# Kernel optimization log

Hardware: AMD Instinct MI355X
Metric: run time of the kernel (lower is better)

Reference implementation:

```python
import jax, jax.numpy as jnp
import numpy as np


def setup_inputs() -> dict:
    key = jax.random.key(0)
    k1, k2, k3, k4 = jax.random.split(key, 4)
    B, L, D, M = 4, 512, 257, 128
    return {
        "input": jax.random.normal(k1, (B, L, 2), dtype=jnp.float32),
        "z0": jax.random.normal(k2, (D,), dtype=jnp.float32),
        "om": jax.random.uniform(k3, (M, 2), dtype=jnp.float32),
        "S": jax.random.normal(k4, (D, D), dtype=jnp.float32),
    }


def _get_T(x, om, S):
    # x: [B, L, 2], om: [M, 2], S: [D, D] with D = 2M+1
    D = S.shape[0]
    M = om.shape[0]
    k_dot_x = jnp.einsum("blc,mc->blm", x, om)          # [B, L, M]
    c = jnp.cos(k_dot_x)
    s = jnp.sin(k_dot_x)
    B, L = x.shape[0], x.shape[1]
    idx1 = 2 * jnp.arange(M) + 1                          # odd indices
    idx2 = idx1 + 1                                       # even indices
    T_irrep = jnp.zeros((B, L, D, D), dtype=x.dtype)
    T_irrep = T_irrep.at[:, :, 0, 0].set(1.0)             # trivial irrep
    T_irrep = T_irrep.at[:, :, idx1, idx1].set(c)
    T_irrep = T_irrep.at[:, :, idx1, idx2].set(-s)
    T_irrep = T_irrep.at[:, :, idx2, idx1].set(s)
    T_irrep = T_irrep.at[:, :, idx2, idx2].set(c)
    S_inv = jnp.linalg.inv(S)
    # T = S @ T_irrep @ S^-1 for every (b, l)
    T = jnp.einsum("ij,bljk,kn->blin", S, T_irrep, S_inv)
    return T


def reference(input, z0, om, S):
    B = input.shape[0]
    T = _get_T(input, om, S)                              # [B, L, D, D]
    z_init = jnp.broadcast_to(z0, (B, z0.shape[0]))       # [B, D]

    def scan_fn(z, T_t):                                  # T_t: [B, D, D]
        z_new = jnp.einsum("bij,bj->bi", T_t, z)
        return z_new, z_new

    _, outs = jax.lax.scan(scan_fn, z_init, jnp.swapaxes(T, 0, 1))  # [L, B, D]
    outputs = jnp.swapaxes(outs, 0, 1)                    # [B, L, D]
    z_final = outputs[:, -1, :]
    return outputs, z_final
```

## Files before the change

kernel.cpp:

```cpp
#include <hip/hip_runtime.h>
#include <math.h>

#define N    257
#define AP   258
#define MM   128
#define LL   512
#define BB   4
#define NB   32
#define U12S 226

#define A_BYTE    0
#define W0_BYTE   530448
#define CXY_BYTE  531488
#define PW_BYTE   547904
#define U12_BYTE  613696
#define ST_BYTE   671552

__global__ __launch_bounds__(512) void stage_scan_kernel(const float* __restrict__ S,
                                                         const float* __restrict__ z0,
                                                         const float* __restrict__ x,
                                                         void* __restrict__ wsv) {
  const int tid = threadIdx.x;
  const int bid = blockIdx.x;

  if (bid < 130) {
    double* A  = (double*)((char*)wsv + A_BYTE);
    float*  St = (float*)((char*)wsv + ST_BYTE);
    const int idx = bid * 512 + tid;
    if (idx < N * N) {
      const int i = idx / N, j = idx - i * N;
      A[(size_t)i * AP + j] = (double)S[idx];
      St[idx] = S[j * N + i];
    } else if (idx < N * N + N) {
      const int r = idx - N * N;
      A[(size_t)r * AP + N] = (double)z0[r];
    }
    return;
  }

  const int wave = tid >> 6, lane = tid & 63;
  const int b    = wave >> 1, comp = wave & 1;
  const float* xp = x + ((size_t)b * LL) * 2 + comp;
  double loc[8];
  double run = 0.0;
  #pragma unroll
  for (int e = 0; e < 8; ++e) {
    run += (double)xp[(lane * 8 + e) * 2];
    loc[e] = run;
  }
  double tot = run;
  #pragma unroll
  for (int off = 1; off < 64; off <<= 1) {
    const double o = __shfl_up(tot, off);
    if (lane >= off) tot += o;
  }
  const double excl = tot - run;
  float* cp = (float*)((char*)wsv + CXY_BYTE) + ((size_t)b * LL) * 2 + comp;
  #pragma unroll
  for (int e = 0; e < 8; ++e)
    cp[(lane * 8 + e) * 2] = (float)(excl + loc[e]);
}

__global__ __launch_bounds__(320, 1) void panel_factor_kernel(void* __restrict__ wsv,
                                                              int k0) {
  __shared__ double piv[2][NB];
  __shared__ double pinvs[2];
  __shared__ double F11s[NB][NB + 1];
  double* A    = (double*)((char*)wsv + A_BYTE);
  double* Pw   = (double*)((char*)wsv + PW_BYTE);
  double* U12w = (double*)((char*)wsv + U12_BYTE);
  const int tid = threadIdx.x;
  const int ct  = k0 + NB;
  const int tc2 = 258 - ct;

  double r[NB];
  if (tid < N) {
    const double* Ar = A + (size_t)tid * AP + k0;
    #pragma unroll
    for (int c = 0; c < NB; c += 2) {
      const double2 v = *(const double2*)&Ar[c];
      r[c] = v.x; r[c + 1] = v.y;
    }
  }

  if (tid == k0) {
    #pragma unroll
    for (int c = 0; c < NB; ++c) piv[0][c] = r[c];
    pinvs[0] = 1.0 / r[0];
  }
  __syncthreads();

  #pragma unroll
  for (int j = 0; j < NB; ++j) {
    const int pr = k0 + j;
    const int bsel = j & 1;
    if (tid < N && (tid < k0 || tid > pr)) {
      const double f = r[j] * pinvs[bsel];
      #pragma unroll
      for (int j2 = j + 1; j2 < NB; ++j2)
        r[j2] -= f * piv[bsel][j2];
      r[j] = f;
      if (j + 1 < NB && tid == pr + 1) {
        #pragma unroll
        for (int c = 0; c < NB; ++c)
          if (c > j) piv[bsel ^ 1][c] = r[c];
        pinvs[bsel ^ 1] = 1.0 / r[j + 1];
      }
    }
    __syncthreads();
  }

  if (tid < N) {
    if (tid >= k0 && tid < ct) {
      const int fr = tid - k0;
      #pragma unroll
      for (int c = 0; c < NB; ++c) {
        F11s[fr][c] = r[c];
        A[(size_t)tid * AP + k0 + c] = r[c];
      }
    } else {
      #pragma unroll
      for (int t = 0; t < NB; ++t)
        Pw[(size_t)t * N + tid] = r[t];
    }
  }
  __syncthreads();

  if (tid < tc2) {
    double u[NB];
    #pragma unroll
    for (int jr = 0; jr < NB; ++jr)
      u[jr] = A[(size_t)(k0 + jr) * AP + ct + tid];
    #pragma unroll
    for (int jr = 1; jr < NB; ++jr) {
      double vv = u[jr];
      #pragma unroll
      for (int t = 0; t < jr; ++t)
        vv -= F11s[jr][t] * u[t];
      u[jr] = vv;
    }
    #pragma unroll
    for (int jr = 0; jr < NB; ++jr) {
      U12w[jr * U12S + tid] = u[jr];
      A[(size_t)(k0 + jr) * AP + ct + tid] = u[jr];
    }
  }
}

__global__ __launch_bounds__(256) void panel_update_kernel(void* __restrict__ wsv,
                                                           int k0, int tc2) {
  __shared__ double Pl[NB][NB + 1];
  __shared__ __align__(16) double Ul[NB][66];
  double* A = (double*)((char*)wsv + A_BYTE);
  const double* Pw   = (const double*)((const char*)wsv + PW_BYTE);
  const double* U12w = (const double*)((const char*)wsv + U12_BYTE);
  const int tid = threadIdx.x;
  const int ct  = k0 + NB;
  const int rb0 = blockIdx.x * 32;
  const int c0  = blockIdx.y * 64;

  for (int i = tid; i < 32 * 32; i += 256) {
    const int t = i >> 5, rr = i & 31;
    const int rb = rb0 + rr;
    const int gr = (rb < k0) ? rb : rb + NB;
    Pl[t][rr] = (rb < 225) ? Pw[(size_t)t * N + gr] : 0.0;
  }
  for (int i = tid; i < 32 * 64; i += 256) {
    const int t = i >> 6, c = i & 63;
    Ul[t][c] = (c0 + c < tc2) ? U12w[t * U12S + c0 + c] : 0.0;
  }
  __syncthreads();

  const int tr  = tid >> 4;
  const int tcx = (tid & 15) * 4;
  double acc[2][4];
  #pragma unroll
  for (int rr = 0; rr < 2; ++rr) {
    const int rb = rb0 + tr * 2 + rr;
    const int gr = (rb < k0) ? rb : rb + NB;
    #pragma unroll
    for (int c = 0; c < 4; ++c)
      acc[rr][c] = (rb < 225 && (c0 + tcx + c) < tc2)
                 ? A[(size_t)gr * AP + ct + c0 + tcx + c] : 0.0;
  }
  #pragma unroll
  for (int t = 0; t < NB; ++t) {
    const double p0 = Pl[t][tr * 2], p1 = Pl[t][tr * 2 + 1];
    const double2 u0 = *(const double2*)&Ul[t][tcx];
    const double2 u1 = *(const double2*)&Ul[t][tcx + 2];
    acc[0][0] -= p0 * u0.x; acc[0][1] -= p0 * u0.y;
    acc[0][2] -= p0 * u1.x; acc[0][3] -= p0 * u1.y;
    acc[1][0] -= p1 * u0.x; acc[1][1] -= p1 * u0.y;
    acc[1][2] -= p1 * u1.x; acc[1][3] -= p1 * u1.y;
  }
  #pragma unroll
  for (int rr = 0; rr < 2; ++rr) {
    const int rb = rb0 + tr * 2 + rr;
    const int gr = (rb < k0) ? rb : rb + NB;
    #pragma unroll
    for (int c = 0; c < 4; ++c)
      if (rb < 225 && (c0 + tcx + c) < tc2)
        A[(size_t)gr * AP + ct + c0 + tcx + c] = acc[rr][c];
  }
}

__global__ __launch_bounds__(256) void last_kernel(void* __restrict__ wsv) {
  __shared__ double xs[N];
  __shared__ double rr[256];
  double* A = (double*)((char*)wsv + A_BYTE);
  const double* Pw   = (const double*)((const char*)wsv + PW_BYTE);
  const double* U12w = (const double*)((const char*)wsv + U12_BYTE);
  float* w0f = (float*)((char*)wsv + W0_BYTE);
  const int tid = threadIdx.x;

  for (int idx = tid; idx < 225 * 2; idx += 256) {
    const int rb = idx >> 1, c = idx & 1;
    const int gr = (rb < 224) ? rb : 256;
    double acc = A[(size_t)gr * AP + 256 + c];
    #pragma unroll
    for (int t = 0; t < NB; ++t)
      acc -= Pw[(size_t)t * N + gr] * U12w[t * U12S + c];
    A[(size_t)gr * AP + 256 + c] = acc;
  }
  __threadfence_block();
  __syncthreads();

  if (tid == 0) xs[256] = A[256 * AP + 257] / A[256 * AP + 256];
  __syncthreads();
  const double x256 = xs[256];
  rr[tid] = A[(size_t)tid * AP + 257] - A[(size_t)tid * AP + 256] * x256;
  __syncthreads();
  const int fk0 = tid & ~31;
  const int fs  = tid & 31;
  for (int j = 31; j >= 0; --j) {
    if (fs == j) xs[fk0 + j] = rr[fk0 + j] / A[(size_t)(fk0 + j) * AP + (fk0 + j)];
    __syncthreads();
    if (fs < j) rr[fk0 + fs] -= A[(size_t)(fk0 + fs) * AP + (fk0 + j)] * xs[fk0 + j];
    __syncthreads();
  }
  w0f[tid] = (float)xs[tid];
  if (tid == 0) w0f[256] = (float)xs[256];
}

#define NL 8
__global__ __launch_bounds__(320) void combine_kernel(const float* __restrict__ S,
                                                      const float* __restrict__ om,
                                                      const void* __restrict__ wsv,
                                                      float* __restrict__ out) {
  const int tid = threadIdx.x;
  const int b  = blockIdx.y;
  const int l0 = blockIdx.x * NL;
  const float* w0  = (const float*)((const char*)wsv + W0_BYTE);
  const float* cxy = (const float*)((const char*)wsv + CXY_BYTE);
  const float* St  = (const float*)((const char*)wsv + ST_BYTE);
  __shared__ __align__(16) float Wl[N][NL];
  __shared__ float omsh[2 * MM];
  __shared__ float cxs[NL], cys[NL];

  for (int idx = tid; idx < 2 * MM; idx += 320) omsh[idx] = om[idx];
  if (tid < NL) {
    cxs[tid] = cxy[((size_t)(b * LL) + l0 + tid) * 2];
    cys[tid] = cxy[((size_t)(b * LL) + l0 + tid) * 2 + 1];
  }
  __syncthreads();

  for (int idx = tid; idx < NL * N; idx += 320) {
    const int d = idx >> 3;
    const int r = idx & 7;
    float v;
    if (d == 0) {
      v = w0[0];
    } else {
      const int m = (d - 1) >> 1;
      const int pq = 2 * m + 1;
      const float t = cxs[r] * omsh[2 * m] + cys[r] * omsh[2 * m + 1];
      float s, c;
      sincosf(t, &s, &c);
      const float a0 = w0[pq], a1 = w0[pq + 1];
      v = (d & 1) ? (c * a0 - s * a1) : (s * a0 + c * a1);
    }
    Wl[d][r] = v;
  }
  __syncthreads();

  const int i = tid;
  if (i < N) {
    float acc[NL];
    #pragma unroll
    for (int r = 0; r < NL; ++r) acc[r] = 0.0f;
    #pragma unroll 8
    for (int d = 0; d < N; ++d) {
      const float stv = St[(size_t)d * N + i];
      const float4 wa = *(const float4*)&Wl[d][0];
      const float4 wb = *(const float4*)&Wl[d][4];
      acc[0] += stv * wa.x; acc[1] += stv * wa.y;
      acc[2] += stv * wa.z; acc[3] += stv * wa.w;
      acc[4] += stv * wb.x; acc[5] += stv * wb.y;
      acc[6] += stv * wb.z; acc[7] += stv * wb.w;
    }
    const size_t base = (size_t)(b * LL + l0) * N + i;
    #pragma unroll
    for (int r = 0; r < NL; ++r) out[base + (size_t)r * N] = acc[r];
    if (l0 + NL == LL) {
      out[(size_t)BB * LL * N + (size_t)b * N + i] = acc[NL - 1];
    }
  }
}

extern "C" void kernel_launch(void* const* d_in, const int* in_sizes, int n_in,
                              void* d_out, int out_size, void* d_ws, size_t ws_size,
                              hipStream_t stream) {
  const float* x  = (const float*)d_in[0];
  const float* z0 = (const float*)d_in[1];
  const float* om = (const float*)d_in[2];
  const float* S  = (const float*)d_in[3];
  float* out = (float*)d_out;

  hipLaunchKernelGGL(stage_scan_kernel, dim3(131), dim3(512), 0, stream, S, z0, x, d_ws);
  for (int p = 0; p < 8; ++p) {
    const int k0  = p * NB;
    const int tc2 = 258 - (k0 + NB);
    hipLaunchKernelGGL(panel_factor_kernel, dim3(1), dim3(320), 0, stream, d_ws, k0);
    if (p < 7)
      hipLaunchKernelGGL(panel_update_kernel, dim3(8, (tc2 + 63) / 64), dim3(256),
                         0, stream, d_ws, k0, tc2);
  }
  hipLaunchKernelGGL(last_kernel, dim3(1), dim3(256), 0, stream, d_ws);
  hipLaunchKernelGGL(combine_kernel, dim3(LL / NL, BB), dim3(320), 0, stream, S, om, d_ws, out);
}
```

Baseline: 345.3 us.

## Factor diagonal panel block with wavefront shuffles instead of per-column block barriers

New measurement: 567.3 us. +64.3%, slower.

```diff
diff --git a/kernel.cpp b/kernel.cpp
--- a/kernel.cpp
+++ b/kernel.cpp
@@ -63,9 +63,8 @@
 
 __global__ __launch_bounds__(320, 1) void panel_factor_kernel(void* __restrict__ wsv,
                                                               int k0) {
-  __shared__ double piv[2][NB];
-  __shared__ double pinvs[2];
   __shared__ double F11s[NB][NB + 1];
+  __shared__ double pinv[NB];
   double* A    = (double*)((char*)wsv + A_BYTE);
   double* Pw   = (double*)((char*)wsv + PW_BYTE);
   double* U12w = (double*)((char*)wsv + U12_BYTE);
@@ -73,9 +72,18 @@
   const int ct  = k0 + NB;
   const int tc2 = 258 - ct;
 
+  int myrow;
+  if (tid < 64) {
+    myrow = k0 + tid;
+  } else {
+    const int rr = tid - 64;
+    myrow = (rr < k0) ? rr : rr + 64;
+  }
+  const bool act = myrow < N;
+
   double r[NB];
-  if (tid < N) {
-    const double* Ar = A + (size_t)tid * AP + k0;
+  if (act) {
+    const double* Ar = A + (size_t)myrow * AP + k0;
     #pragma unroll
     for (int c = 0; c < NB; c += 2) {
       const double2 v = *(const double2*)&Ar[c];
@@ -83,66 +91,64 @@
     }
   }
 
-  if (tid == k0) {
-    #pragma unroll
-    for (int c = 0; c < NB; ++c) piv[0][c] = r[c];
-    pinvs[0] = 1.0 / r[0];
-  }
-  __syncthreads();
-
-  #pragma unroll
-  for (int j = 0; j < NB; ++j) {
-    const int pr = k0 + j;
-    const int bsel = j & 1;
-    if (tid < N && (tid < k0 || tid > pr)) {
-      const double f = r[j] * pinvs[bsel];
+  if (tid < 64) {
+    #pragma unroll
+    for (int j = 0; j < NB; ++j) {
+      const double ujj = __shfl(r[j], j);
+      const double pj  = 1.0 / ujj;
+      const double m   = r[j] * pj;
+      #pragma unroll
+      for (int j2 = j + 1; j2 < NB; ++j2) {
+        const double uv = __shfl(r[j2], j);
+        if (tid > j && act) r[j2] -= m * uv;
+      }
+      if (tid > j && act) r[j] = m;
+    }
+    if (tid < NB) {
+      #pragma unroll
+      for (int c = 0; c < NB; ++c) {
+        F11s[tid][c] = r[c];
+        A[(size_t)(k0 + tid) * AP + k0 + c] = r[c];
+      }
+      pinv[tid] = 1.0 / r[tid];
+    } else if (act) {
+      #pragma unroll
+      for (int t = 0; t < NB; ++t)
+        Pw[(size_t)t * N + myrow] = r[t];
+    }
+  }
+  __syncthreads();
+
+  if (tid >= 64 && act) {
+    #pragma unroll
+    for (int j = 0; j < NB; ++j) {
+      const double f = r[j] * pinv[j];
       #pragma unroll
       for (int j2 = j + 1; j2 < NB; ++j2)
-        r[j2] -= f * piv[bsel][j2];
+        r[j2] -= f * F11s[j][j2];
       r[j] = f;
-      if (j + 1 < NB && tid == pr + 1) {
-        #pragma unroll
-        for (int c = 0; c < NB; ++c)
-          if (c > j) piv[bsel ^ 1][c] = r[c];
-        pinvs[bsel ^ 1] = 1.0 / r[j + 1];
-      }
-    }
-    __syncthreads();
-  }
-
-  if (tid < N) {
-    if (tid >= k0 && tid < ct) {
-      const int fr = tid - k0;
-      #pragma unroll
-      for (int c = 0; c < NB; ++c) {
-        F11s[fr][c] = r[c];
-        A[(size_t)tid * AP + k0 + c] = r[c];
-      }
-    } else {
-      #pragma unroll
-      for (int t = 0; t < NB; ++t)
-        Pw[(size_t)t * N + tid] = r[t];
-    }
-  }
-  __syncthreads();
+    }
+    #pragma unroll
+    for (int t = 0; t < NB; ++t)
+      Pw[(size_t)t * N + myrow] = r[t];
+  }
 
   if (tid < tc2) {
-    double u[NB];
     #pragma unroll
     for (int jr = 0; jr < NB; ++jr)
-      u[jr] = A[(size_t)(k0 + jr) * AP + ct + tid];
+      r[jr] = A[(size_t)(k0 + jr) * AP + ct + tid];
     #pragma unroll
     for (int jr = 1; jr < NB; ++jr) {
-      double vv = u[jr];
+      double vv = r[jr];
       #pragma unroll
       for (int t = 0; t < jr; ++t)
-        vv -= F11s[jr][t] * u[t];
-      u[jr] = vv;
+        vv -= F11s[jr][t] * r[t];
+      r[jr] = vv;
     }
     #pragma unroll
     for (int jr = 0; jr < NB; ++jr) {
-      U12w[jr * U12S + tid] = u[jr];
-      A[(size_t)(k0 + jr) * AP + ct + tid] = u[jr];
+      U12w[jr * U12S + tid] = r[jr];
+      A[(size_t)(k0 + jr) * AP + ct + tid] = r[jr];
     }
   }
 }
```
